# Optimization experiments

Measured on AMD Instinct MI355X. Metric: run time of the kernel, lower is better.

## Reference

```python
import jax, jax.numpy as jnp
import numpy as np

DIM = 64
SQRT_DIM = float(np.sqrt(DIM))


def setup_inputs() -> dict:
    key = jax.random.key(0)
    k1, k2, k3, k4 = jax.random.split(key, 4)
    B, S, D = 32, 2048, DIM
    query = jax.random.normal(k1, (B, S, D), dtype=jnp.float32)
    key_t = jax.random.normal(k2, (B, S, D), dtype=jnp.float32)
    value = jax.random.normal(k3, (B, S, D), dtype=jnp.float32)
    mask = jax.random.randint(k4, (B, S, S), 0, 2).astype(jnp.bool_)
    return {"query": query, "key": key_t, "value": value, "mask": mask}


def reference(query, key, value, mask):
    # score: [B, S, S]
    score = jnp.einsum('bqd,bkd->bqk', query, key) / SQRT_DIM
    score = jnp.where(mask, -jnp.inf, score)
    attn = jax.nn.softmax(score, axis=-1)
    # fully-masked rows produce NaN in softmax; torch.nan_to_num -> 0
    attn = jnp.nan_to_num(attn, nan=0.0)
    context = jnp.einsum('bqk,bkd->bqd', attn, value)
    return context
```

## Files before the change

### kernel.cpp

```cpp
#include <hip/hip_runtime.h>
#include <hip/hip_bf16.h>

#define BATCH 32
#define SEQ   2048
#define DIM   64
#define KT    64
#define NIT   (SEQ / KT)
#define QTB   256

typedef __attribute__((ext_vector_type(8))) short bf16x8;
typedef __attribute__((ext_vector_type(4))) short bf16x4;
typedef __attribute__((ext_vector_type(4))) float fx4;
typedef __attribute__((ext_vector_type(4))) int   ix4;

static __device__ __forceinline__ short f2bf(float f) {
    __bf16 h = (__bf16)f;
    return *(short*)&h;
}
static __device__ __forceinline__ bf16x4 cvt4(float a, float b, float c, float d) {
    bf16x4 s; s[0] = f2bf(a); s[1] = f2bf(b); s[2] = f2bf(c); s[3] = f2bf(d);
    return s;
}

#define QSCALE (0.125f * 1.44269504088896f)

__global__ __launch_bounds__(1024, 4)
void attn_fwd(const float* __restrict__ Qg, const float* __restrict__ Kg,
              const float* __restrict__ Vg, const int* __restrict__ Mg,
              float* __restrict__ Og)
{
    __shared__ __align__(16) char smem[32768];

    const int bid   = (int)((blockIdx.x & 7) * 32 + (blockIdx.x >> 3));
    const int b     = bid >> 3;
    const int qbase = (bid & 7) * QTB;
    const int tid   = threadIdx.x;
    const int wave  = tid >> 6;
    const int lane  = tid & 63;
    const int l15   = lane & 15;
    const int g     = lane >> 4;

    const int qrow_g = qbase + wave * 16 + l15;
    const float* qrow = Qg + ((size_t)(b * SEQ + qrow_g) * DIM);
    bf16x8 qf[2];
#pragma unroll
    for (int h = 0; h < 2; ++h) {
        fx4 a = *(const fx4*)(qrow + h * 32 + g * 8);
        fx4 c = *(const fx4*)(qrow + h * 32 + g * 8 + 4);
        a *= QSCALE; c *= QSCALE;
        bf16x8 q;
        q[0]=f2bf(a[0]); q[1]=f2bf(a[1]); q[2]=f2bf(a[2]); q[3]=f2bf(a[3]);
        q[4]=f2bf(c[0]); q[5]=f2bf(c[1]); q[6]=f2bf(c[2]); q[7]=f2bf(c[3]);
        qf[h] = q;
    }

    const int* mrow = Mg + ((size_t)(b * SEQ + qrow_g) * SEQ) + 4 * g;

    const int kr = tid >> 4, kcq = tid & 15;
    const float* ksrc = Kg + ((size_t)(b * SEQ + kr) * DIM) + kcq * 4;
    const int kwofs = kr * 128 + ((kcq * 8) ^ ((kr & 7) * 16));

    const int vd = tid & 63, jg = tid >> 6;
    const float* vsrc = Vg + ((size_t)(b * SEQ + jg * 4) * DIM) + vd;
    const int vpr = vd >> 1, vu = vd & 1, jg7 = jg & 7;
    const int vwofs = 16384 + (jg >> 3) * 4096 + vpr * 128 +
                      (((vu * 64) + 16 * (jg7 & 3) + 8 * (jg7 >> 2)) ^ ((vpr & 7) * 16));

    const int ksw  = (l15 & 7) * 16;
    const int koh0 = l15 * 128 + ((16 * g)      ^ ksw);
    const int koh1 = l15 * 128 + ((16 * g + 64) ^ ksw);
    const int vrof = (l15 >> 1) * 128 + (((l15 & 1) * 64 + 16 * g) ^ ((l15 >> 1) * 16));

    fx4 acc[4] = {};
    float lsum = 0.f;

    fx4   kReg[2];
    float vReg[2][4];
    ix4   m[4];

    {
        fx4 k0 = *(const fx4*)(ksrc);
        float v0[4];
#pragma unroll
        for (int i = 0; i < 4; ++i) v0[i] = vsrc[(size_t)i * DIM];
        kReg[0] = *(const fx4*)(ksrc + (size_t)KT * DIM);
#pragma unroll
        for (int i = 0; i < 4; ++i) vReg[0][i] = vsrc[(size_t)(KT + i) * DIM];
#pragma unroll
        for (int s = 0; s < 4; ++s)
            m[s] = __builtin_nontemporal_load((const ix4*)(mrow + s * 16));
        *(bf16x4*)(smem + kwofs) = cvt4(k0[0], k0[1], k0[2], k0[3]);
        *(bf16x4*)(smem + vwofs) = cvt4(v0[0], v0[1], v0[2], v0[3]);
    }
    asm volatile("s_waitcnt lgkmcnt(0)" ::: "memory");
    __builtin_amdgcn_s_barrier();
    __builtin_amdgcn_sched_barrier(0);

#pragma unroll 2
    for (int kt = 0; kt < NIT; ++kt) {
        const int cur = kt & 1, nxt = cur ^ 1;
        const int kb2 = ((kt + 2) & (NIT - 1)) * KT;
        const int kb1 = ((kt + 1) & (NIT - 1)) * KT;

        kReg[nxt] = *(const fx4*)(ksrc + (size_t)kb2 * DIM);
#pragma unroll
        for (int i = 0; i < 4; ++i) vReg[nxt][i] = vsrc[(size_t)(kb2 + i) * DIM];

        const char* kB = smem + cur * 8192;
        fx4 sc[4];
#pragma unroll
        for (int s = 0; s < 4; ++s) {
            bf16x8 kf0 = *(const bf16x8*)(kB + s * 2048 + koh0);
            bf16x8 kf1 = *(const bf16x8*)(kB + s * 2048 + koh1);
            fx4 t = {};
            t = __builtin_amdgcn_mfma_f32_16x16x32_bf16(kf0, qf[0], t, 0, 0, 0);
            t = __builtin_amdgcn_mfma_f32_16x16x32_bf16(kf1, qf[1], t, 0, 0, 0);
            sc[s] = t;
        }

        float p[16];
#pragma unroll
        for (int s = 0; s < 4; ++s)
#pragma unroll
            for (int i = 0; i < 4; ++i)
                p[s * 4 + i] = m[s][i] ? 0.f : __builtin_amdgcn_exp2f(sc[s][i]);
#pragma unroll
        for (int s = 0; s < 4; ++s)
            m[s] = __builtin_nontemporal_load((const ix4*)(mrow + kb1 + s * 16));

        lsum += (((p[0] + p[1]) + (p[2] + p[3])) + ((p[4] + p[5]) + (p[6] + p[7])))
              + (((p[8] + p[9]) + (p[10] + p[11])) + ((p[12] + p[13]) + (p[14] + p[15])));

        bf16x8 pf0, pf1;
#pragma unroll
        for (int j = 0; j < 8; ++j) { pf0[j] = f2bf(p[j]); pf1[j] = f2bf(p[8 + j]); }

        const char* vB = smem + 16384 + cur * 8192 + vrof;
#pragma unroll
        for (int dsub = 0; dsub < 4; ++dsub) {
            bf16x8 vf = *(const bf16x8*)(vB + dsub * 1024);
            acc[dsub] = __builtin_amdgcn_mfma_f32_16x16x32_bf16(vf, pf0, acc[dsub], 0, 0, 0);
        }
#pragma unroll
        for (int dsub = 0; dsub < 4; ++dsub) {
            bf16x8 vf = *(const bf16x8*)(vB + 4096 + dsub * 1024);
            acc[dsub] = __builtin_amdgcn_mfma_f32_16x16x32_bf16(vf, pf1, acc[dsub], 0, 0, 0);
        }

        *(bf16x4*)(smem + nxt * 8192 + kwofs) =
            cvt4(kReg[cur][0], kReg[cur][1], kReg[cur][2], kReg[cur][3]);
        *(bf16x4*)(smem + nxt * 8192 + vwofs) =
            cvt4(vReg[cur][0], vReg[cur][1], vReg[cur][2], vReg[cur][3]);

        asm volatile("s_waitcnt lgkmcnt(0)" ::: "memory");
        __builtin_amdgcn_s_barrier();
        __builtin_amdgcn_sched_barrier(0);
    }

    lsum += __shfl_xor(lsum, 16);
    lsum += __shfl_xor(lsum, 32);
    const float inv = lsum > 0.f ? 1.0f / lsum : 0.f;

    float* obase = Og + ((size_t)(b * SEQ + qrow_g) * DIM) + 4 * g;
#pragma unroll
    for (int dsub = 0; dsub < 4; ++dsub) {
        fx4 o = acc[dsub] * inv;
        __builtin_nontemporal_store(o, (fx4*)(obase + dsub * 16));
    }
}

extern "C" void kernel_launch(void* const* d_in, const int* in_sizes, int n_in,
                              void* d_out, int out_size, void* d_ws, size_t ws_size,
                              hipStream_t stream) {
    const float* Q = (const float*)d_in[0];
    const float* K = (const float*)d_in[1];
    const float* V = (const float*)d_in[2];
    const int*   M = (const int*)d_in[3];
    float*       O = (float*)d_out;
    dim3 grid(BATCH * (SEQ / QTB));
    attn_fwd<<<grid, 1024, 0, stream>>>(Q, K, V, M, O);
}
```

Measured before the change: 136.3 us.

## Load mask rows coalesced and compress to ballot bitmasks per 256-key superblock

Instead of each lane loading its own strided slice of the mask row, each wave now loads whole 256-key mask row segments contiguously across lanes. It packs them via __ballot into 64-bit bitmasks, which are distributed to the owning lane with selects. Masks for the next superblock are prefetched four rows per iteration and swapped in every four tiles. The aim is more coalesced mask traffic, which dominates bandwidth, and fewer mask registers, at the cost of extra ballot and select ALU work and a loop unrolled by four.

Result: no change. 135.5 us (-0.6%).

```diff
diff --git a/kernel.cpp b/kernel.cpp
--- a/kernel.cpp
+++ b/kernel.cpp
@@ -7,6 +7,7 @@
 #define KT    64
 #define NIT   (SEQ / KT)
 #define QTB   256
+#define NSUP  (NIT / 4)
 
 typedef __attribute__((ext_vector_type(8))) short bf16x8;
 typedef __attribute__((ext_vector_type(4))) short bf16x4;
@@ -54,7 +55,7 @@
         qf[h] = q;
     }
 
-    const int* mrow = Mg + ((size_t)(b * SEQ + qrow_g) * SEQ) + 4 * g;
+    const int* mload = Mg + ((size_t)(b * SEQ + qbase + wave * 16) * SEQ) + 4 * lane;
 
     const int kr = tid >> 4, kcq = tid & 15;
     const float* ksrc = Kg + ((size_t)(b * SEQ + kr) * DIM) + kcq * 4;
@@ -76,7 +77,8 @@
 
     fx4   kReg[2];
     float vReg[2][4];
-    ix4   m[4];
+    unsigned long long vselA[4] = {0, 0, 0, 0};
+    unsigned long long vselB[4] = {0, 0, 0, 0};
 
     {
         fx4 k0 = *(const fx4*)(ksrc);
@@ -86,21 +88,42 @@
         kReg[0] = *(const fx4*)(ksrc + (size_t)KT * DIM);
 #pragma unroll
         for (int i = 0; i < 4; ++i) vReg[0][i] = vsrc[(size_t)(KT + i) * DIM];
-#pragma unroll
-        for (int s = 0; s < 4; ++s)
-            m[s] = __builtin_nontemporal_load((const ix4*)(mrow + s * 16));
         *(bf16x4*)(smem + kwofs) = cvt4(k0[0], k0[1], k0[2], k0[3]);
         *(bf16x4*)(smem + vwofs) = cvt4(v0[0], v0[1], v0[2], v0[3]);
+#pragma unroll
+        for (int h = 0; h < 2; ++h) {
+            ix4 mm8[8];
+#pragma unroll
+            for (int r = 0; r < 8; ++r)
+                mm8[r] = __builtin_nontemporal_load(
+                    (const ix4*)(mload + (size_t)(h * 8 + r) * SEQ));
+#pragma unroll
+            for (int r = 0; r < 8; ++r) {
+                const bool sel = (l15 == h * 8 + r);
+#pragma unroll
+                for (int i = 0; i < 4; ++i) {
+                    unsigned long long W = __ballot(mm8[r][i] != 0);
+                    vselA[i] = sel ? W : vselA[i];
+                }
+            }
+        }
     }
     asm volatile("s_waitcnt lgkmcnt(0)" ::: "memory");
     __builtin_amdgcn_s_barrier();
     __builtin_amdgcn_sched_barrier(0);
 
-#pragma unroll 2
+#pragma unroll 4
     for (int kt = 0; kt < NIT; ++kt) {
+        const int tp  = kt & 3;
         const int cur = kt & 1, nxt = cur ^ 1;
-        const int kb2 = ((kt + 2) & (NIT - 1)) * KT;
-        const int kb1 = ((kt + 1) & (NIT - 1)) * KT;
+        const int kb2  = ((kt + 2) & (NIT - 1)) * KT;
+        const int mofs = ((((kt >> 2) + 1) & (NSUP - 1)) * 256);
+
+        ix4 mm[4];
+#pragma unroll
+        for (int u = 0; u < 4; ++u)
+            mm[u] = __builtin_nontemporal_load(
+                (const ix4*)(mload + (size_t)(4 * tp + u) * SEQ + mofs));
 
         kReg[nxt] = *(const fx4*)(ksrc + (size_t)kb2 * DIM);
 #pragma unroll
@@ -120,13 +143,13 @@
 
         float p[16];
 #pragma unroll
-        for (int s = 0; s < 4; ++s)
-#pragma unroll
-            for (int i = 0; i < 4; ++i)
-                p[s * 4 + i] = m[s][i] ? 0.f : __builtin_amdgcn_exp2f(sc[s][i]);
-#pragma unroll
-        for (int s = 0; s < 4; ++s)
-            m[s] = __builtin_nontemporal_load((const ix4*)(mrow + kb1 + s * 16));
+        for (int i = 0; i < 4; ++i) {
+            const unsigned long long w = vselA[i] >> g;
+            p[0 + i]  = ((w >> (16 * tp + 0))  & 1ull) ? 0.f : __builtin_amdgcn_exp2f(sc[0][i]);
+            p[4 + i]  = ((w >> (16 * tp + 4))  & 1ull) ? 0.f : __builtin_amdgcn_exp2f(sc[1][i]);
+            p[8 + i]  = ((w >> (16 * tp + 8))  & 1ull) ? 0.f : __builtin_amdgcn_exp2f(sc[2][i]);
+            p[12 + i] = ((w >> (16 * tp + 12)) & 1ull) ? 0.f : __builtin_amdgcn_exp2f(sc[3][i]);
+        }
 
         lsum += (((p[0] + p[1]) + (p[2] + p[3])) + ((p[4] + p[5]) + (p[6] + p[7])))
               + (((p[8] + p[9]) + (p[10] + p[11])) + ((p[12] + p[13]) + (p[14] + p[15])));
@@ -151,6 +174,23 @@
             cvt4(kReg[cur][0], kReg[cur][1], kReg[cur][2], kReg[cur][3]);
         *(bf16x4*)(smem + nxt * 8192 + vwofs) =
             cvt4(vReg[cur][0], vReg[cur][1], vReg[cur][2], vReg[cur][3]);
+
+        {
+            const int rbase = 4 * tp;
+#pragma unroll
+            for (int u = 0; u < 4; ++u) {
+                const bool sel = (l15 == rbase + u);
+#pragma unroll
+                for (int i = 0; i < 4; ++i) {
+                    unsigned long long W = __ballot(mm[u][i] != 0);
+                    vselB[i] = sel ? W : vselB[i];
+                }
+            }
+        }
+        if (tp == 3) {
+            vselA[0] = vselB[0]; vselA[1] = vselB[1];
+            vselA[2] = vselB[2]; vselA[3] = vselB[3];
+        }
 
         asm volatile("s_waitcnt lgkmcnt(0)" ::: "memory");
         __builtin_amdgcn_s_barrier();
```
